# Optimization experiments

Measured on AMD Instinct MI355X. Metric: run time of the kernel, lower is better.

The kernel has to match this reference:

```python
import jax, jax.numpy as jnp
import numpy as np

BS = 256
HID = 1024
ACT = 16
MEM_DIM = 512
NUM_MEM = 1024
MEM_H = 32  # sqrt(NUM_MEM)
ALPHA_T = 1.0


def setup_inputs() -> dict:
    key = jax.random.key(0)
    ks = jax.random.split(key, 16)
    w = lambda i, shape: (jax.random.normal(ks[i], shape, jnp.float32) * 0.02)
    inp = {
        "h": jax.random.normal(ks[0], (BS, HID), jnp.float32),
        "a": jax.random.uniform(ks[1], (BS, ACT), jnp.float32),
        "prev_h": jax.random.normal(ks[2], (BS, HID), jnp.float32),
        "prev_alpha": jax.random.uniform(ks[3], (BS, NUM_MEM), jnp.float32),
        "M": jax.random.normal(ks[4], (BS, NUM_MEM, MEM_DIM), jnp.float32) * 0.05,
        # get_vars_h: Linear(HID, 3*MEM_DIM)
        "Wv": w(5, (HID, 3 * MEM_DIM)), "bv": jnp.zeros((3 * MEM_DIM,), jnp.float32),
        # get_kernel: Linear(ACT, MEM_DIM) -> LeakyReLU(0.2) -> Linear(MEM_DIM, 9)
        "Wk1": w(6, (ACT, MEM_DIM)), "bk1": jnp.zeros((MEM_DIM,), jnp.float32),
        "Wk2": w(7, (MEM_DIM, 9)), "bk2": jnp.zeros((9,), jnp.float32),
        # get_gate: Linear(HID, MEM_DIM) -> LeakyReLU(0.2) -> Linear(MEM_DIM, 1) -> Sigmoid
        "Wg1": w(8, (HID, MEM_DIM)), "bg1": jnp.zeros((MEM_DIM,), jnp.float32),
        "Wg2": w(9, (MEM_DIM, 1)), "bg2": jnp.zeros((1,), jnp.float32),
    }
    return inp


def _kernel_net(x, Wk1, bk1, Wk2, bk2):
    # [bs, ACT] -> [bs, 1, 3, 3]
    k = jax.nn.leaky_relu(x @ Wk1 + bk1, 0.2) @ Wk2 + bk2
    return k.reshape(-1, 1, 3, 3)


def _dyn_conv(prev_alpha, kernels):
    # per-sample 3x3 conv: input [1, bs, 32, 32], kernel [bs, 1, 3, 3], groups=bs
    x = prev_alpha.reshape(1, BS, MEM_H, MEM_H)
    out = jax.lax.conv_general_dilated(
        x, kernels, window_strides=(1, 1), padding="SAME",
        dimension_numbers=("NCHW", "OIHW", "NCHW"), feature_group_count=BS)
    return out.reshape(BS, NUM_MEM)


def reference(h, a, prev_h, prev_alpha, M,
              Wv, bv, Wk1, bk1, Wk2, bk2, Wg1, bg1, Wg2, bg2):
    # mem_use_h=True -> memory query input is h (prev_h unused)
    kernels = _kernel_net(a, Wk1, bk1, Wk2, bk2)

    # vizdoom action masking (vectorized): if argmax(a)==0 -> a[1]=1, a[0]=0
    m = jnp.argmax(a, axis=1) == 0  # [bs]
    new_a = a.at[:, 0].set(jnp.where(m, 0.0, a[:, 0]))
    new_a = new_a.at[:, 1].set(jnp.where(m, 1.0, new_a[:, 1]))
    flipped = _kernel_net(new_a, Wk1, bk1, Wk2, bk2)[:, :, ::-1, ::-1]
    maskf = m.astype(jnp.float32)[:, None, None, None]
    kernels = (1.0 - maskf) * kernels + maskf * flipped

    # softmax_kernel=True
    kernels = jax.nn.softmax(kernels.reshape(BS, 9) / ALPHA_T, axis=1)
    kernels = kernels.reshape(BS, 1, 3, 3)

    gate = jax.nn.sigmoid(jax.nn.leaky_relu(h @ Wg1 + bg1, 0.2) @ Wg2 + bg2)  # [bs,1]

    alpha = _dyn_conv(prev_alpha, kernels)           # [bs, NUM_MEM]
    alpha = alpha * gate + prev_alpha * (1.0 - gate)

    # write (read_only=False)
    tmp = h @ Wv + bv                                 # [bs, 3*MEM_DIM]
    erase_v = jax.nn.sigmoid(tmp[:, :MEM_DIM])
    add_v = tmp[:, MEM_DIM:2 * MEM_DIM]
    other_v = tmp[:, 2 * MEM_DIM:]
    erase = alpha[:, :, None] * erase_v[:, None, :]   # [bs, NUM_MEM, MEM_DIM]
    add = alpha[:, :, None] * add_v[:, None, :]
    M_new = M * (1.0 - erase) + add

    read_v = jnp.einsum("bn,bnd->bd", alpha, M_new)   # [bs, MEM_DIM]
    return read_v, other_v, M_new, alpha
```

## Files before the change

kernel.cpp:

```cpp
#include <hip/hip_runtime.h>
#include <math.h>

#define BS 256
#define HID 1024
#define ACT 16
#define MEM_DIM 512
#define NUM_MEM 1024
#define MEM_H 32

#define OUT_READV 0
#define OUT_OTHER (BS * MEM_DIM)
#define OUT_MNEW  (2 * BS * MEM_DIM)
#define OUT_ALPHA (2 * BS * MEM_DIM + (size_t)BS * NUM_MEM * MEM_DIM)

#define WS_ERASE 0
#define WS_ADD   (BS * MEM_DIM)
#define WS_G1    (2 * BS * MEM_DIM)

typedef float v4f __attribute__((ext_vector_type(4)));

__device__ __forceinline__ float sigmoidf_(float x) { return 1.f / (1.f + expf(-x)); }
__device__ __forceinline__ float leakyf_(float x) { return x > 0.f ? x : 0.2f * x; }

#define TM 32
#define TN 64
#define KC 32

__global__ __launch_bounds__(256) void gemm_fused_kernel(
    const float* __restrict__ h, const float* __restrict__ Wv,
    const float* __restrict__ Wg1, const float* __restrict__ bv,
    const float* __restrict__ bg1, float* __restrict__ ws,
    float* __restrict__ out_other)
{
    __shared__ float As[KC][TM + 1];
    __shared__ float Bs[KC][TN + 4];
    int tid = threadIdx.x;
    int n0 = blockIdx.x * TN;
    int m0 = blockIdx.y * TM;
    int tc = tid & 15, tr = tid >> 4;

    float acc[2][4];
    #pragma unroll
    for (int j = 0; j < 2; ++j)
        #pragma unroll
        for (int i = 0; i < 4; ++i) acc[j][i] = 0.f;

    int a_m  = tid >> 3;
    int a_k4 = (tid & 7) * 4;
    int b_n4 = (tid & 15) * 4;
    int b_k  = tid >> 4;
    const bool isWv = (n0 < 3 * MEM_DIM);

    for (int k0 = 0; k0 < HID; k0 += KC) {
        float4 av4 = *(const float4*)&h[(size_t)(m0 + a_m) * HID + k0 + a_k4];
        As[a_k4 + 0][a_m] = av4.x;
        As[a_k4 + 1][a_m] = av4.y;
        As[a_k4 + 2][a_m] = av4.z;
        As[a_k4 + 3][a_m] = av4.w;
        #pragma unroll
        for (int p = 0; p < 2; ++p) {
            int kk = b_k + p * 16;
            float4 bv4;
            if (isWv)
                bv4 = *(const float4*)&Wv[(size_t)(k0 + kk) * (3 * MEM_DIM) + n0 + b_n4];
            else
                bv4 = *(const float4*)&Wg1[(size_t)(k0 + kk) * MEM_DIM + (n0 - 3 * MEM_DIM) + b_n4];
            *(float4*)&Bs[kk][b_n4] = bv4;
        }
        __syncthreads();
        #pragma unroll
        for (int k = 0; k < KC; ++k) {
            float a0 = As[k][tr * 2 + 0];
            float a1 = As[k][tr * 2 + 1];
            float4 b4 = *(float4*)&Bs[k][tc * 4];
            acc[0][0] += a0 * b4.x; acc[0][1] += a0 * b4.y;
            acc[0][2] += a0 * b4.z; acc[0][3] += a0 * b4.w;
            acc[1][0] += a1 * b4.x; acc[1][1] += a1 * b4.y;
            acc[1][2] += a1 * b4.z; acc[1][3] += a1 * b4.w;
        }
        __syncthreads();
    }

    int seg = n0 >> 9;
    #pragma unroll
    for (int j = 0; j < 2; ++j) {
        int r = m0 + tr * 2 + j;
        #pragma unroll
        for (int i = 0; i < 4; ++i) {
            int c = n0 + tc * 4 + i;
            float v = acc[j][i];
            if (seg < 3) v += bv[c]; else v += bg1[c - 3 * MEM_DIM];
            if (seg == 0)      ws[WS_ERASE + r * MEM_DIM + c]               = sigmoidf_(v);
            else if (seg == 1) ws[WS_ADD   + r * MEM_DIM + (c - MEM_DIM)]   = v;
            else if (seg == 2) out_other[r * MEM_DIM + (c - 2 * MEM_DIM)]   = v;
            else               ws[WS_G1    + r * MEM_DIM + (c - 3 * MEM_DIM)] = leakyf_(v);
        }
    }
}

__global__ __launch_bounds__(256) void update_fused_kernel(
    const float* __restrict__ a, const float* __restrict__ Wk1,
    const float* __restrict__ bk1, const float* __restrict__ Wk2,
    const float* __restrict__ bk2,
    const float* __restrict__ prev_alpha,
    const float* __restrict__ g1, const float* __restrict__ Wg2,
    const float* __restrict__ bg2,
    const float* __restrict__ M,
    const float* __restrict__ erase, const float* __restrict__ add,
    float* __restrict__ M_new, float* __restrict__ read_v,
    float* __restrict__ alpha_out)
{
    int b  = blockIdx.x;
    int dc = blockIdx.y;
    int t  = threadIdx.x;

    __shared__ __align__(16) float pa[NUM_MEM];
    __shared__ __align__(16) float al[NUM_MEM];
    __shared__ float ksh[9];
    __shared__ float gsh;

    int dl = (t & 31) * 4;
    int d  = dc * 128 + dl;
    v4f e  = *(const v4f*)(erase + b * MEM_DIM + d);
    v4f ad = *(const v4f*)(add   + b * MEM_DIM + d);

    if (t < 64) {
        float as_[ACT];
        #pragma unroll
        for (int j = 0; j < ACT; ++j) as_[j] = a[b * ACT + j];
        float mx = as_[1];
        #pragma unroll
        for (int j = 2; j < ACT; ++j) mx = fmaxf(mx, as_[j]);
        bool m = as_[0] >= mx;

        float po[9], pn[9];
        #pragma unroll
        for (int o = 0; o < 9; ++o) { po[o] = 0.f; pn[o] = 0.f; }

        #pragma unroll
        for (int i = 0; i < 8; ++i) {
            int u = t + 64 * i;
            float so = bk1[u], sn = bk1[u];
            #pragma unroll
            for (int j = 0; j < ACT; ++j) {
                float w  = Wk1[j * MEM_DIM + u];
                float av = as_[j];
                float avn = (j == 0) ? (m ? 0.f : av)
                          : (j == 1) ? (m ? 1.f : av) : av;
                so += av * w;
                sn += avn * w;
            }
            so = leakyf_(so);
            sn = leakyf_(sn);
            #pragma unroll
            for (int o = 0; o < 9; ++o) {
                float w2 = Wk2[u * 9 + o];
                po[o] += so * w2;
                pn[o] += sn * w2;
            }
        }
        #pragma unroll
        for (int off = 32; off; off >>= 1) {
            #pragma unroll
            for (int o = 0; o < 9; ++o) {
                po[o] += __shfl_down(po[o], off, 64);
                pn[o] += __shfl_down(pn[o], off, 64);
            }
        }
        if (t == 0) {
            float k[9];
            #pragma unroll
            for (int o = 0; o < 9; ++o) {
                float ko = po[o] + bk2[o];
                float kn = pn[8 - o] + bk2[8 - o];
                k[o] = m ? kn : ko;
            }
            float kmax = k[0];
            #pragma unroll
            for (int o = 1; o < 9; ++o) kmax = fmaxf(kmax, k[o]);
            float s = 0.f;
            #pragma unroll
            for (int o = 0; o < 9; ++o) { k[o] = expf(k[o] - kmax); s += k[o]; }
            float inv = 1.f / s;
            #pragma unroll
            for (int o = 0; o < 9; ++o) ksh[o] = k[o] * inv;
        }
    } else if (t < 128) {
        int l = t - 64;
        float p = 0.f;
        #pragma unroll
        for (int k = 0; k < 8; ++k)
            p += g1[b * MEM_DIM + l + 64 * k] * Wg2[l + 64 * k];
        #pragma unroll
        for (int off = 32; off; off >>= 1) p += __shfl_down(p, off, 64);
        if (l == 0) gsh = sigmoidf_(p + bg2[0]);
    } else {
        int i0 = (t - 128) * 8;
        *(float4*)&pa[i0]     = *(const float4*)&prev_alpha[(size_t)b * NUM_MEM + i0];
        *(float4*)&pa[i0 + 4] = *(const float4*)&prev_alpha[(size_t)b * NUM_MEM + i0 + 4];
    }
    __syncthreads();

    float gate = gsh;
    v4f outv;
    #pragma unroll
    for (int q = 0; q < 4; ++q) {
        int c = t * 4 + q;
        int i = c >> 5, j = c & 31;
        float s = 0.f;
        #pragma unroll
        for (int ki = 0; ki < 3; ++ki) {
            int ii = i + ki - 1;
            if (ii < 0 || ii >= MEM_H) continue;
            #pragma unroll
            for (int kj = 0; kj < 3; ++kj) {
                int jj = j + kj - 1;
                if (jj < 0 || jj >= MEM_H) continue;
                s += pa[ii * MEM_H + jj] * ksh[ki * 3 + kj];
            }
        }
        float v = s * gate + pa[c] * (1.f - gate);
        al[c] = v;
        outv[q] = v;
    }
    if (dc == 0)
        *(v4f*)&alpha_out[(size_t)b * NUM_MEM + t * 4] = outv;
    __syncthreads();

    const float* Mb = M     + (size_t)b * NUM_MEM * MEM_DIM + d;
    float*       Ob = M_new + (size_t)b * NUM_MEM * MEM_DIM + d;
    const float* alp = &al[(t >> 5) * 128];
    Mb += (size_t)(t >> 5) * 128 * MEM_DIM;
    Ob += (size_t)(t >> 5) * 128 * MEM_DIM;

    v4f acc = 0.f;
    #pragma unroll 8
    for (int i = 0; i < 128; ++i) {
        float av = alp[i];
        v4f m4 = __builtin_nontemporal_load((const v4f*)(Mb + (size_t)i * MEM_DIM));
        v4f mn = m4 * (1.f - av * e) + av * ad;
        __builtin_nontemporal_store(mn, (v4f*)(Ob + (size_t)i * MEM_DIM));
        acc += av * mn;
    }

    *(v4f*)&pa[t * 4] = acc;
    __syncthreads();
    if (t < 32) {
        v4f s = *(v4f*)&pa[t * 4];
        #pragma unroll
        for (int j = 1; j < 8; ++j) s += *(v4f*)&pa[(t + 32 * j) * 4];
        *(v4f*)(read_v + (size_t)b * MEM_DIM + dc * 128 + t * 4) = s;
    }
}

extern "C" void kernel_launch(void* const* d_in, const int* in_sizes, int n_in,
                              void* d_out, int out_size, void* d_ws, size_t ws_size,
                              hipStream_t stream)
{
    const float* h          = (const float*)d_in[0];
    const float* a          = (const float*)d_in[1];
    const float* prev_alpha = (const float*)d_in[3];
    const float* M          = (const float*)d_in[4];
    const float* Wv         = (const float*)d_in[5];
    const float* bv         = (const float*)d_in[6];
    const float* Wk1        = (const float*)d_in[7];
    const float* bk1        = (const float*)d_in[8];
    const float* Wk2        = (const float*)d_in[9];
    const float* bk2        = (const float*)d_in[10];
    const float* Wg1        = (const float*)d_in[11];
    const float* bg1        = (const float*)d_in[12];
    const float* Wg2        = (const float*)d_in[13];
    const float* bg2        = (const float*)d_in[14];

    float* out = (float*)d_out;
    float* ws  = (float*)d_ws;

    float* out_readv = out + OUT_READV;
    float* out_other = out + OUT_OTHER;
    float* out_mnew  = out + OUT_MNEW;
    float* out_alpha = out + OUT_ALPHA;

    gemm_fused_kernel<<<dim3(2048 / TN, BS / TM), 256, 0, stream>>>(
        h, Wv, Wg1, bv, bg1, ws, out_other);

    update_fused_kernel<<<dim3(BS, 4), 256, 0, stream>>>(
        a, Wk1, bk1, Wk2, bk2, prev_alpha,
        ws + WS_G1, Wg2, bg2, M,
        ws + WS_ERASE, ws + WS_ADD,
        out_mnew, out_readv, out_alpha);
}
```

Measured before the change: 960.5 us.

## Use one 512-thread block per batch row to drop redundant alpha recomputation

The update kernel now launches one 512-thread block per batch sample instead of four 256-thread blocks that each covered a 128-column slice of MEM_DIM. The kernel-net, gate and 3x3 convolution for alpha are computed once per sample rather than four times. Each group of 128 threads now streams full 512-wide memory rows, interleaving rows across the four groups. The change also cuts the grid from 1024 to 256 blocks, which lowers the number of blocks in flight for this memory-bound streaming of M.

```diff
diff --git a/kernel.cpp b/kernel.cpp
--- a/kernel.cpp
+++ b/kernel.cpp
@@ -98,7 +98,7 @@
     }
 }
 
-__global__ __launch_bounds__(256) void update_fused_kernel(
+__global__ __launch_bounds__(512) void update_fused_kernel(
     const float* __restrict__ a, const float* __restrict__ Wk1,
     const float* __restrict__ bk1, const float* __restrict__ Wk2,
     const float* __restrict__ bk2,
@@ -110,17 +110,15 @@
     float* __restrict__ M_new, float* __restrict__ read_v,
     float* __restrict__ alpha_out)
 {
-    int b  = blockIdx.x;
-    int dc = blockIdx.y;
-    int t  = threadIdx.x;
+    int b = blockIdx.x;
+    int t = threadIdx.x;
 
     __shared__ __align__(16) float pa[NUM_MEM];
     __shared__ __align__(16) float al[NUM_MEM];
     __shared__ float ksh[9];
     __shared__ float gsh;
 
-    int dl = (t & 31) * 4;
-    int d  = dc * 128 + dl;
+    int d = (t & 127) * 4;
     v4f e  = *(const v4f*)(erase + b * MEM_DIM + d);
     v4f ad = *(const v4f*)(add   + b * MEM_DIM + d);
 
@@ -194,7 +192,7 @@
         #pragma unroll
         for (int off = 32; off; off >>= 1) p += __shfl_down(p, off, 64);
         if (l == 0) gsh = sigmoidf_(p + bg2[0]);
-    } else {
+    } else if (t < 256) {
         int i0 = (t - 128) * 8;
         *(float4*)&pa[i0]     = *(const float4*)&prev_alpha[(size_t)b * NUM_MEM + i0];
         *(float4*)&pa[i0 + 4] = *(const float4*)&prev_alpha[(size_t)b * NUM_MEM + i0 + 4];
@@ -202,54 +200,54 @@
     __syncthreads();
 
     float gate = gsh;
-    v4f outv;
-    #pragma unroll
-    for (int q = 0; q < 4; ++q) {
-        int c = t * 4 + q;
-        int i = c >> 5, j = c & 31;
-        float s = 0.f;
-        #pragma unroll
-        for (int ki = 0; ki < 3; ++ki) {
-            int ii = i + ki - 1;
-            if (ii < 0 || ii >= MEM_H) continue;
-            #pragma unroll
-            for (int kj = 0; kj < 3; ++kj) {
-                int jj = j + kj - 1;
-                if (jj < 0 || jj >= MEM_H) continue;
-                s += pa[ii * MEM_H + jj] * ksh[ki * 3 + kj];
-            }
-        }
-        float v = s * gate + pa[c] * (1.f - gate);
-        al[c] = v;
-        outv[q] = v;
-    }
-    if (dc == 0)
+    if (t < 256) {
+        v4f outv;
+        #pragma unroll
+        for (int q = 0; q < 4; ++q) {
+            int c = t * 4 + q;
+            int i = c >> 5, j = c & 31;
+            float s = 0.f;
+            #pragma unroll
+            for (int ki = 0; ki < 3; ++ki) {
+                int ii = i + ki - 1;
+                if (ii < 0 || ii >= MEM_H) continue;
+                #pragma unroll
+                for (int kj = 0; kj < 3; ++kj) {
+                    int jj = j + kj - 1;
+                    if (jj < 0 || jj >= MEM_H) continue;
+                    s += pa[ii * MEM_H + jj] * ksh[ki * 3 + kj];
+                }
+            }
+            float v = s * gate + pa[c] * (1.f - gate);
+            al[c] = v;
+            outv[q] = v;
+        }
         *(v4f*)&alpha_out[(size_t)b * NUM_MEM + t * 4] = outv;
-    __syncthreads();
-
-    const float* Mb = M     + (size_t)b * NUM_MEM * MEM_DIM + d;
-    float*       Ob = M_new + (size_t)b * NUM_MEM * MEM_DIM + d;
-    const float* alp = &al[(t >> 5) * 128];
-    Mb += (size_t)(t >> 5) * 128 * MEM_DIM;
-    Ob += (size_t)(t >> 5) * 128 * MEM_DIM;
+    }
+    __syncthreads();
+
+    int g = t >> 7;
+    const float* Mb = M     + (size_t)b * NUM_MEM * MEM_DIM + (size_t)g * MEM_DIM + d;
+    float*       Ob = M_new + (size_t)b * NUM_MEM * MEM_DIM + (size_t)g * MEM_DIM + d;
 
     v4f acc = 0.f;
     #pragma unroll 8
-    for (int i = 0; i < 128; ++i) {
-        float av = alp[i];
-        v4f m4 = __builtin_nontemporal_load((const v4f*)(Mb + (size_t)i * MEM_DIM));
+    for (int i = 0; i < 256; ++i) {
+        float av = al[g + i * 4];
+        v4f m4 = __builtin_nontemporal_load((const v4f*)(Mb + (size_t)i * 4 * MEM_DIM));
         v4f mn = m4 * (1.f - av * e) + av * ad;
-        __builtin_nontemporal_store(mn, (v4f*)(Ob + (size_t)i * MEM_DIM));
+        __builtin_nontemporal_store(mn, (v4f*)(Ob + (size_t)i * 4 * MEM_DIM));
         acc += av * mn;
     }
 
-    *(v4f*)&pa[t * 4] = acc;
-    __syncthreads();
-    if (t < 32) {
-        v4f s = *(v4f*)&pa[t * 4];
-        #pragma unroll
-        for (int j = 1; j < 8; ++j) s += *(v4f*)&pa[(t + 32 * j) * 4];
-        *(v4f*)(read_v + (size_t)b * MEM_DIM + dc * 128 + t * 4) = s;
+    __syncthreads();
+    if (t < 256) *(v4f*)&pa[t * 4]         = acc;
+    else         *(v4f*)&al[(t - 256) * 4] = acc;
+    __syncthreads();
+    if (t < 128) {
+        v4f s = *(v4f*)&pa[t * 4] + *(v4f*)&pa[(t + 128) * 4]
+              + *(v4f*)&al[t * 4] + *(v4f*)&al[(t + 128) * 4];
+        *(v4f*)(read_v + (size_t)b * MEM_DIM + t * 4) = s;
     }
 }
 
@@ -283,7 +281,7 @@
     gemm_fused_kernel<<<dim3(2048 / TN, BS / TM), 256, 0, stream>>>(
         h, Wv, Wg1, bv, bg1, ws, out_other);
 
-    update_fused_kernel<<<dim3(BS, 4), 256, 0, stream>>>(
+    update_fused_kernel<<<BS, 512, 0, stream>>>(
         a, Wk1, bk1, Wk2, bk2, prev_alpha,
         ws + WS_G1, Wg2, bg2, M,
         ws + WS_ERASE, ws + WS_ADD,
```

Result: faster. 931.5 us (-3.0%).
